# Kernel tuning notes

Hardware: AMD Instinct MI355X
Metric: run time of the kernel (lower is better)

Reference implementation:

```python
import jax, jax.numpy as jnp
import numpy as np

VOCAB = 50257
D_MODEL = 1024
SEQ_LEN = 2048
BATCH = 16
WIDTH_MULT = 8.0
MAX_TOKEN_SIZE = 20  # rows >= this are zeroed every forward (hard-coded in source)


def setup_inputs() -> dict:
    key = jax.random.key(0)
    k1, k2 = jax.random.split(key)
    x = jax.random.randint(k1, (SEQ_LEN, BATCH), 0, VOCAB)  # (L, B) token ids
    # 'mup' init: randn(fan_in, fan_out) * width_mult ** -0.5
    embed_w = jax.random.normal(k2, (VOCAB, D_MODEL), dtype=jnp.float32) * (WIDTH_MULT ** -0.5)
    return {"x": x, "embed_w": embed_w}


def reference(x, embed_w):
    # Source zeroes embedding rows >= MAX_TOKEN_SIZE in-place (no_grad), then
    # does one-hot @ embed_w, which is exactly a row gather. We gather directly
    # (same math, no O(vocab) dense GEMM).
    w = embed_w.at[MAX_TOKEN_SIZE:, :].set(0.0)
    emb = jnp.take(w, x, axis=0)               # (L, B, D)
    out = jnp.transpose(emb, (1, 2, 0))         # (B, D, L) per 'bdl' einsum output
    return out * (WIDTH_MULT ** 0.5)            # 'mup' output multiplier
```

## Files before the change

kernel.cpp:

```cpp
#include <hip/hip_runtime.h>


constexpr int D_MODEL = 1024;
constexpr int SEQ_LEN = 2048;
constexpr int BATCH   = 16;
constexpr int MAXTOK  = 20;
constexpr int LPB     = 256;
constexpr int DPB     = 32;
__device__ constexpr float SCALE = 2.8284271247461903f;

__global__ __launch_bounds__(256) void embed_gather_kernel(
    const int* __restrict__ x,
    const float* __restrict__ w,
    float* __restrict__ out)
{
    const int b    = blockIdx.x;
    const int lc   = blockIdx.y;
    const int dc   = blockIdx.z;
    const int lane = threadIdx.x & 63;
    const int wv   = threadIdx.x >> 6;

    const int l0 = lc * LPB + lane * 4;
    const int d0 = dc * DPB + wv * 8;

    const int tok0 = x[(l0 + 0) * BATCH + b];
    const int tok1 = x[(l0 + 1) * BATCH + b];
    const int tok2 = x[(l0 + 2) * BATCH + b];
    const int tok3 = x[(l0 + 3) * BATCH + b];

    const bool live0 = tok0 < MAXTOK;
    const bool live1 = tok1 < MAXTOK;
    const bool live2 = tok2 < MAXTOK;
    const bool live3 = tok3 < MAXTOK;
    const bool any   = live0 | live1 | live2 | live3;

    float* outp = out + ((size_t)b * D_MODEL + d0) * SEQ_LEN + l0;

    if (!any) {
        const float4 z = make_float4(0.f, 0.f, 0.f, 0.f);
        #pragma unroll
        for (int i = 0; i < 8; ++i) {
            *reinterpret_cast<float4*>(outp) = z;
            outp += SEQ_LEN;
        }
    } else {
        const float* w0 = w + (size_t)tok0 * D_MODEL + d0;
        const float* w1 = w + (size_t)tok1 * D_MODEL + d0;
        const float* w2 = w + (size_t)tok2 * D_MODEL + d0;
        const float* w3 = w + (size_t)tok3 * D_MODEL + d0;
        #pragma unroll
        for (int i = 0; i < 8; ++i) {
            float4 v;
            v.x = live0 ? w0[i] * SCALE : 0.f;
            v.y = live1 ? w1[i] * SCALE : 0.f;
            v.z = live2 ? w2[i] * SCALE : 0.f;
            v.w = live3 ? w3[i] * SCALE : 0.f;
            *reinterpret_cast<float4*>(outp) = v;
            outp += SEQ_LEN;
        }
    }
}

extern "C" void kernel_launch(void* const* d_in, const int* in_sizes, int n_in,
                              void* d_out, int out_size, void* d_ws, size_t ws_size,
                              hipStream_t stream) {
    const int*   x = (const int*)d_in[0];
    const float* w = (const float*)d_in[1];
    float*     out = (float*)d_out;

    dim3 grid(BATCH, SEQ_LEN / LPB, D_MODEL / DPB);
    dim3 block(256);
    embed_gather_kernel<<<grid, block, 0, stream>>>(x, w, out);
}
```

Baseline: 281.9 us.

## Zero output with memset and scatter only live-token rows via ballot

Replaces the full gather kernel with a hipMemsetAsync that zeroes the whole output, followed by a scatter kernel. The scatter kernel uses a wavefront ballot to find tokens below the live threshold and writes only their scaled embedding rows. The aim is to avoid reading embedding rows and computing per-element selects for the mostly dead tokens, relying on memset's fast fill. In exchange it adds a second launch, and the live-row writes are strided by SEQ_LEN, so they are uncoalesced.

```diff
diff --git a/kernel.cpp b/kernel.cpp
--- a/kernel.cpp
+++ b/kernel.cpp
@@ -5,58 +5,34 @@
 constexpr int SEQ_LEN = 2048;
 constexpr int BATCH   = 16;
 constexpr int MAXTOK  = 20;
-constexpr int LPB     = 256;
-constexpr int DPB     = 32;
 __device__ constexpr float SCALE = 2.8284271247461903f;
 
-__global__ __launch_bounds__(256) void embed_gather_kernel(
+__global__ __launch_bounds__(256) void embed_scatter_kernel(
     const int* __restrict__ x,
     const float* __restrict__ w,
     float* __restrict__ out)
 {
-    const int b    = blockIdx.x;
-    const int lc   = blockIdx.y;
-    const int dc   = blockIdx.z;
+    const int idx  = blockIdx.x * 256 + threadIdx.x;
     const int lane = threadIdx.x & 63;
-    const int wv   = threadIdx.x >> 6;
 
-    const int l0 = lc * LPB + lane * 4;
-    const int d0 = dc * DPB + wv * 8;
+    const int tok   = x[idx];
+    const bool live = tok < MAXTOK;
 
-    const int tok0 = x[(l0 + 0) * BATCH + b];
-    const int tok1 = x[(l0 + 1) * BATCH + b];
-    const int tok2 = x[(l0 + 2) * BATCH + b];
-    const int tok3 = x[(l0 + 3) * BATCH + b];
+    unsigned long long m = __ballot(live);
+    while (m) {
+        const int src = __ffsll(m) - 1;
+        m &= m - 1;
+        const int t  = __shfl(tok, src);
+        const int si = __shfl(idx, src);
+        const int l  = si >> 4;
+        const int b  = si & (BATCH - 1);
 
-    const bool live0 = tok0 < MAXTOK;
-    const bool live1 = tok1 < MAXTOK;
-    const bool live2 = tok2 < MAXTOK;
-    const bool live3 = tok3 < MAXTOK;
-    const bool any   = live0 | live1 | live2 | live3;
-
-    float* outp = out + ((size_t)b * D_MODEL + d0) * SEQ_LEN + l0;
-
-    if (!any) {
-        const float4 z = make_float4(0.f, 0.f, 0.f, 0.f);
+        const float* wp = w + (size_t)t * D_MODEL;
+        float* op = out + (size_t)b * D_MODEL * SEQ_LEN + l;
         #pragma unroll
-        for (int i = 0; i < 8; ++i) {
-            *reinterpret_cast<float4*>(outp) = z;
-            outp += SEQ_LEN;
-        }
-    } else {
-        const float* w0 = w + (size_t)tok0 * D_MODEL + d0;
-        const float* w1 = w + (size_t)tok1 * D_MODEL + d0;
-        const float* w2 = w + (size_t)tok2 * D_MODEL + d0;
-        const float* w3 = w + (size_t)tok3 * D_MODEL + d0;
-        #pragma unroll
-        for (int i = 0; i < 8; ++i) {
-            float4 v;
-            v.x = live0 ? w0[i] * SCALE : 0.f;
-            v.y = live1 ? w1[i] * SCALE : 0.f;
-            v.z = live2 ? w2[i] * SCALE : 0.f;
-            v.w = live3 ? w3[i] * SCALE : 0.f;
-            *reinterpret_cast<float4*>(outp) = v;
-            outp += SEQ_LEN;
+        for (int k = 0; k < D_MODEL / 64; ++k) {
+            const int d = k * 64 + lane;
+            op[(size_t)d * SEQ_LEN] = wp[d] * SCALE;
         }
     }
 }
@@ -68,7 +44,10 @@
     const float* w = (const float*)d_in[1];
     float*     out = (float*)d_out;
 
-    dim3 grid(BATCH, SEQ_LEN / LPB, D_MODEL / DPB);
+    hipMemsetAsync(out, 0, (size_t)BATCH * D_MODEL * SEQ_LEN * sizeof(float), stream);
+
+    const int total = SEQ_LEN * BATCH;
+    dim3 grid(total / 256);
     dim3 block(256);
-    embed_gather_kernel<<<grid, block, 0, stream>>>(x, w, out);
+    embed_scatter_kernel<<<grid, block, 0, stream>>>(x, w, out);
 }
```

Result: faster. 273.0 us (-3.1%).
